# Optimization experiments

Measured on AMD Instinct MI355X. Metric: run time of the kernel, lower is better.

## Reference

```python
import jax, jax.numpy as jnp
import numpy as np

N_NODES = 50000
N_EDGES = 1600000
HIDDEN = 1024
NUM_CLASSES = 64


def setup_inputs() -> dict:
    key = jax.random.key(0)
    k1, k2, k3 = jax.random.split(key, 3)
    x = jax.random.normal(k1, (N_NODES, HIDDEN), dtype=jnp.float32)
    edge_index = jax.random.randint(k2, (2, N_EDGES), 0, N_NODES, dtype=jnp.int64)
    # Glorot-style init for the GCNConv linear weight, zero bias (PyG defaults)
    W = jax.random.normal(k3, (HIDDEN, NUM_CLASSES), dtype=jnp.float32) / np.sqrt(HIDDEN)
    b = jnp.zeros((NUM_CLASSES,), dtype=jnp.float32)
    return {"x": x, "edge_index": edge_index, "W": W, "b": b}


def reference(x, edge_index, W, b):
    # GCNConv: add self-loops, symmetric deg^{-1/2} normalization,
    # linear transform, gather-scale-scatter aggregation, bias, then softmax.
    n = x.shape[0]
    loops = jnp.arange(n, dtype=edge_index.dtype)
    src = jnp.concatenate([edge_index[0], loops])  # [E+N]
    dst = jnp.concatenate([edge_index[1], loops])  # [E+N]

    ones = jnp.ones(dst.shape[0], dtype=x.dtype)
    deg = jax.ops.segment_sum(ones, dst, num_segments=n)  # in-degree incl. self-loop
    deg_inv_sqrt = jnp.where(deg > 0, jax.lax.rsqrt(deg), 0.0)
    norm = deg_inv_sqrt[src] * deg_inv_sqrt[dst]  # [E+N]

    h = x @ W  # [N, C] dense GEMM (transform before propagate)
    msgs = h[src] * norm[:, None]  # gather + scale
    out = jax.ops.segment_sum(msgs, dst, num_segments=n) + b  # scatter-add
    return jax.nn.softmax(out, axis=1)
```

## Files before the change

kernel.cpp:

```cpp
#include <hip/hip_runtime.h>
#include <hip/hip_bf16.h>
#include <hip/hip_fp16.h>
#include <math.h>

#define HIDDEN 1024
#define NCLS 64
#define NB 196
#define BCAP 10240
#define CHUNK 4096
#define GCAP 4096
#define SMEM_BYTES 33280

typedef __attribute__((ext_vector_type(8))) short short8;
typedef __attribute__((ext_vector_type(4))) float f32x4;
typedef __attribute__((ext_vector_type(8))) _Float16 half8;

__device__ __forceinline__ short f2bf(float f) {
    __hip_bfloat16 b = __float2bfloat16(f);
    return __builtin_bit_cast(short, b);
}
__device__ __forceinline__ float bf2f(short s) {
    unsigned u = ((unsigned)(unsigned short)s) << 16;
    return __builtin_bit_cast(float, u);
}

__device__ __forceinline__ void async_copy16(void* lds, const void* g) {
    __builtin_amdgcn_global_load_lds(
        (const __attribute__((address_space(1))) unsigned int*)g,
        (__attribute__((address_space(3))) unsigned int*)lds, 16, 0, 0);
}

__global__ void wprep_kernel(const float* __restrict__ W,
                             short* __restrict__ wt_hi, short* __restrict__ wt_lo) {
    int idx = blockIdx.x * 256 + threadIdx.x;
    int c = idx >> 10;
    int k = idx & 1023;
    float f = W[(size_t)k * NCLS + c];
    short hb = f2bf(f);
    wt_hi[idx] = hb;
    wt_lo[idx] = f2bf(f - bf2f(hb));
}

__device__ void bucket_body(char* smem, const int* __restrict__ ei,
                            unsigned* __restrict__ pairs, int* __restrict__ bcnt,
                            int E, int bid) {
    int* hist = (int*)smem;
    int* offs = hist + 256;
    int* cur  = offs + 256;
    int* gbase = cur + 256;
    unsigned* stage = (unsigned*)(gbase + 256);
    int* nz = (int*)(stage + CHUNK);
    int* wsum = nz + 1;

    const int tid = threadIdx.x;
    const int base = bid * CHUNK;
    const int cnt_c = min(CHUNK, E - base);

    if (tid == 0) *nz = 0;
    hist[tid] = 0;
    cur[tid] = 0;
    __syncthreads();

    int found = 0;
    for (int j = tid; j < 1024; j += 256) {
        int e = base + j;
        if (e < E) found |= (ei[2 * e + 1] != 0);
    }
    if (found) atomicOr(nz, 1);
    __syncthreads();
    const int is64 = (*nz == 0);

    unsigned pr[16];
    #pragma unroll
    for (int j = 0; j < 16; ++j) {
        int e = base + j * 256 + tid;
        unsigned p = 0xFFFFFFFFu;
        if (e < E) {
            int s = is64 ? ei[2 * e] : ei[e];
            int d = is64 ? ei[2 * (E + e)] : ei[E + e];
            p = (unsigned)s | ((unsigned)d << 16);
            atomicAdd(&hist[d >> 8], 1);
        }
        pr[j] = p;
    }
    __syncthreads();

    int v = hist[tid];
    int incl = v;
    #pragma unroll
    for (int d = 1; d < 64; d <<= 1) {
        int t = __shfl_up(incl, d);
        if ((tid & 63) >= d) incl += t;
    }
    if ((tid & 63) == 63) wsum[tid >> 6] = incl;
    __syncthreads();
    int pre = 0;
    #pragma unroll
    for (int w = 0; w < 4; ++w)
        if (w < (tid >> 6)) pre += wsum[w];
    offs[tid] = pre + incl - v;
    if (tid < NB && v > 0) gbase[tid] = atomicAdd(&bcnt[tid], v);
    __syncthreads();

    #pragma unroll
    for (int j = 0; j < 16; ++j) {
        unsigned p = pr[j];
        if (p != 0xFFFFFFFFu) {
            int b = (int)(p >> 24);
            int pos = offs[b] + atomicAdd(&cur[b], 1);
            stage[pos] = p;
        }
    }
    __syncthreads();
    for (int i = tid; i < cnt_c; i += 256) {
        unsigned p = stage[i];
        int b = (int)(p >> 24);
        pairs[(size_t)b * BCAP + gbase[b] + (i - offs[b])] = p;
    }
}

__device__ void gemm_body(char* smem, const float* __restrict__ x,
                          const short* __restrict__ wt_hi, const short* __restrict__ wt_lo,
                          _Float16* __restrict__ h16, int M, int bid) {
    char* As = smem;
    char* Bh = smem + 16 * 1040;
    char* Bl = smem + 24 * 1040;

    const int tid = threadIdx.x;
    const int wave = tid >> 6;
    const int lane = tid & 63;
    const int l15 = lane & 15, l4 = lane >> 4;
    const int row0 = bid * 64;

    const float* agp[4];
    #pragma unroll
    for (int i = 0; i < 4; ++i) {
        int rg = row0 + (wave * 4 + i) * 4 + (lane >> 4);
        if (rg > M - 1) rg = M - 1;
        int g = (lane & 15) ^ (((lane >> 4) & 3) << 2);
        agp[i] = x + (size_t)rg * HIDDEN + g * 4;
    }
    const short* bhp[2];
    const short* blp[2];
    #pragma unroll
    for (int i = 0; i < 2; ++i) {
        int c = (wave * 2 + i) * 8 + (lane >> 3);
        int g = (lane & 7) ^ ((lane >> 3) & 7);
        bhp[i] = wt_hi + (size_t)c * HIDDEN + g * 8;
        blp[i] = wt_lo + (size_t)c * HIDDEN + g * 8;
    }

    f32x4 acc[4];
    #pragma unroll
    for (int nf = 0; nf < 4; ++nf) acc[nf] = (f32x4){0.f, 0.f, 0.f, 0.f};

    const int rt = wave * 16 + l15;
    const int r3 = rt & 3;
    char* arow = As + (rt >> 2) * 1040 + r3 * 256;

    for (int k0 = 0; k0 < HIDDEN; k0 += 64) {
        #pragma unroll
        for (int i = 0; i < 4; ++i)
            async_copy16(As + (wave * 4 + i) * 1040, agp[i] + k0);
        #pragma unroll
        for (int i = 0; i < 2; ++i) {
            async_copy16(Bh + (wave * 2 + i) * 1040, bhp[i] + k0);
            async_copy16(Bl + (wave * 2 + i) * 1040, blp[i] + k0);
        }
        __syncthreads();

        #pragma unroll
        for (int kk = 0; kk < 2; ++kk) {
            int js = (kk * 8 + l4 * 2) ^ (r3 << 2);
            f32x4 af0 = *reinterpret_cast<const f32x4*>(arow + js * 16);
            f32x4 af1 = *reinterpret_cast<const f32x4*>(arow + js * 16 + 16);
            short8 ah, al;
            #pragma unroll
            for (int j = 0; j < 4; ++j) {
                short hb = f2bf(af0[j]);
                ah[j] = hb;
                al[j] = f2bf(af0[j] - bf2f(hb));
                short hb2 = f2bf(af1[j]);
                ah[j + 4] = hb2;
                al[j + 4] = f2bf(af1[j] - bf2f(hb2));
            }
            #pragma unroll
            for (int nf = 0; nf < 4; ++nf) {
                int c = l15 + 16 * nf;
                int jb = (kk * 4 + l4) ^ (c & 7);
                size_t boff = (size_t)(c >> 3) * 1040 + (c & 7) * 128 + jb * 16;
                short8 bh = *reinterpret_cast<const short8*>(Bh + boff);
                short8 bl = *reinterpret_cast<const short8*>(Bl + boff);
                acc[nf] = __builtin_amdgcn_mfma_f32_16x16x32_bf16(ah, bh, acc[nf], 0, 0, 0);
                acc[nf] = __builtin_amdgcn_mfma_f32_16x16x32_bf16(al, bh, acc[nf], 0, 0, 0);
                acc[nf] = __builtin_amdgcn_mfma_f32_16x16x32_bf16(ah, bl, acc[nf], 0, 0, 0);
            }
        }
        __syncthreads();
    }

    #pragma unroll
    for (int j = 0; j < 4; ++j) {
        int r = row0 + wave * 16 + l4 * 4 + j;
        if (r < M) {
            #pragma unroll
            for (int nf = 0; nf < 4; ++nf) {
                h16[(size_t)r * NCLS + l15 + 16 * nf] = (_Float16)acc[nf][j];
            }
        }
    }
}

__global__ __launch_bounds__(256) void fat_kernel(const float* __restrict__ x,
                                                  const short* __restrict__ wt_hi,
                                                  const short* __restrict__ wt_lo,
                                                  _Float16* __restrict__ h16, int M,
                                                  const int* __restrict__ ei,
                                                  unsigned* __restrict__ pairs,
                                                  int* __restrict__ bcnt, int E,
                                                  int nGemmBlocks) {
    __shared__ __align__(16) char smem[SMEM_BYTES];
    if ((int)blockIdx.x < nGemmBlocks)
        gemm_body(smem, x, wt_hi, wt_lo, h16, M, blockIdx.x);
    else
        bucket_body(smem, ei, pairs, bcnt, E, blockIdx.x - nGemmBlocks);
}

__global__ __launch_bounds__(256) void degree_kernel(const unsigned* __restrict__ pairs,
                                                     const int* __restrict__ bcnt,
                                                     float* __restrict__ dis, int n) {
    __shared__ int hist[256];
    const int tid = threadIdx.x;
    const int bucket = blockIdx.x;
    hist[tid] = 0;
    __syncthreads();
    const int cb = bcnt[bucket];
    const unsigned* bp = pairs + (size_t)bucket * BCAP;
    for (int i = tid; i < cb; i += 256) {
        unsigned p = bp[i];
        atomicAdd(&hist[(p >> 16) & 255], 1);
    }
    __syncthreads();
    int node = bucket * 256 + tid;
    if (node < n) dis[node] = rsqrtf((float)hist[tid] + 1.0f);
}

__global__ __launch_bounds__(256) void agg_kernel(const unsigned* __restrict__ pairs,
                                                  const int* __restrict__ bcnt,
                                                  const _Float16* __restrict__ h16,
                                                  const float* __restrict__ dis,
                                                  const float* __restrict__ bias,
                                                  float* __restrict__ out, int n) {
    __shared__ int hist[64];
    __shared__ int offs[64];
    __shared__ int cur[64];
    __shared__ unsigned short ssrc[GCAP];
    __shared__ float swt[GCAP];
    const int tid = threadIdx.x;
    const int bucket = blockIdx.x >> 2;
    const int split = blockIdx.x & 3;
    const int base_node = bucket * 256 + split * 64;
    if (base_node >= n) return;
    if (tid < 64) { hist[tid] = 0; cur[tid] = 0; }
    __syncthreads();
    const int cb = bcnt[bucket];
    const unsigned* bp = pairs + (size_t)bucket * BCAP;
    for (int i = tid; i < cb; i += 256) {
        unsigned p = bp[i];
        int loc = (int)((p >> 16) & 255u);
        if ((loc >> 6) == split) atomicAdd(&hist[loc & 63], 1);
    }
    __syncthreads();
    if (tid == 0) {
        int r = 0;
        #pragma unroll
        for (int k = 0; k < 64; ++k) { offs[k] = r; r += hist[k]; }
    }
    __syncthreads();
    for (int i = tid; i < cb; i += 256) {
        unsigned p = bp[i];
        int loc = (int)((p >> 16) & 255u);
        if ((loc >> 6) == split) {
            int ln = loc & 63;
            int pos = offs[ln] + atomicAdd(&cur[ln], 1);
            if (pos < GCAP) {
                int s = (int)(p & 0xFFFFu);
                ssrc[pos] = (unsigned short)s;
                swt[pos] = dis[s];
            }
        }
    }
    __syncthreads();

    const int wave = tid >> 6;
    const int lane = tid & 63;
    const int q = lane & 7;
    const int g = lane >> 3;
    float bv[8];
    #pragma unroll
    for (int c = 0; c < 8; ++c) bv[c] = bias[q * 8 + c];

    for (int t = 0; t < 16; ++t) {
        int ln = wave * 16 + t;
        int node = base_node + ln;
        if (node >= n) continue;
        int len = hist[ln];
        int e0 = offs[ln];
        float di = rsqrtf((float)len + 1.0f);

        half8 hs = *reinterpret_cast<const half8*>(h16 + (size_t)node * NCLS + q * 8);
        float selfw = (g == 0) ? di : 0.f;
        float a[8], a2[8];
        #pragma unroll
        for (int c = 0; c < 8; ++c) { a[c] = (float)hs[c] * selfw; a2[c] = 0.f; }

        for (int i = 0; i < len; i += 16) {
            int i1 = i + g;
            bool v1 = i1 < len;
            int s1 = v1 ? (int)ssrc[e0 + i1] : 0;
            float w1 = v1 ? swt[e0 + i1] : 0.f;
            half8 r1 = *reinterpret_cast<const half8*>(h16 + (size_t)s1 * NCLS + q * 8);
            if (i + 8 < len) {
                int i2 = i + 8 + g;
                bool v2 = i2 < len;
                int s2 = v2 ? (int)ssrc[e0 + i2] : 0;
                float w2 = v2 ? swt[e0 + i2] : 0.f;
                half8 r2 = *reinterpret_cast<const half8*>(h16 + (size_t)s2 * NCLS + q * 8);
                #pragma unroll
                for (int c = 0; c < 8; ++c) a2[c] += w2 * (float)r2[c];
            }
            #pragma unroll
            for (int c = 0; c < 8; ++c) a[c] += w1 * (float)r1[c];
        }
        #pragma unroll
        for (int c = 0; c < 8; ++c) {
            float s = a[c] + a2[c];
            s += __shfl_xor(s, 8);
            s += __shfl_xor(s, 16);
            s += __shfl_xor(s, 32);
            a[c] = s * di + bv[c];
        }
        float m = a[0];
        #pragma unroll
        for (int c = 1; c < 8; ++c) m = fmaxf(m, a[c]);
        #pragma unroll
        for (int d = 1; d < 8; d <<= 1) m = fmaxf(m, __shfl_xor(m, d));
        float ex[8], sum = 0.f;
        #pragma unroll
        for (int c = 0; c < 8; ++c) { ex[c] = __expf(a[c] - m); sum += ex[c]; }
        #pragma unroll
        for (int d = 1; d < 8; d <<= 1) sum += __shfl_xor(sum, d);
        float inv = 1.f / sum;
        if (g == 0) {
            f32x4 o0 = {ex[0] * inv, ex[1] * inv, ex[2] * inv, ex[3] * inv};
            f32x4 o1 = {ex[4] * inv, ex[5] * inv, ex[6] * inv, ex[7] * inv};
            *reinterpret_cast<f32x4*>(out + (size_t)node * NCLS + q * 8) = o0;
            *reinterpret_cast<f32x4*>(out + (size_t)node * NCLS + q * 8 + 4) = o1;
        }
    }
}

extern "C" void kernel_launch(void* const* d_in, const int* in_sizes, int n_in,
                              void* d_out, int out_size, void* d_ws, size_t ws_size,
                              hipStream_t stream) {
    const float* x    = (const float*)d_in[0];
    const int*   ei   = (const int*)d_in[1];
    const float* W    = (const float*)d_in[2];
    const float* bias = (const float*)d_in[3];
    float* out = (float*)d_out;

    const int n = in_sizes[0] / HIDDEN;
    const int E = in_sizes[1] / 2;

    char* ws = (char*)d_ws;
    size_t off = 0;
    auto alloc = [&](size_t bytes) -> void* {
        void* p = (void*)(ws + off);
        off = (off + bytes + 255) & ~((size_t)255);
        return p;
    };
    int*      bcnt  = (int*)alloc((size_t)NB * 4);
    unsigned* pairs = (unsigned*)alloc((size_t)NB * BCAP * 4);
    float*    dis   = (float*)alloc((size_t)n * 4);
    _Float16* h16   = (_Float16*)alloc((size_t)n * NCLS * 2);
    short*    wt_hi = (short*)alloc((size_t)NCLS * HIDDEN * 2);
    short*    wt_lo = (short*)alloc((size_t)NCLS * HIDDEN * 2);
    (void)ws_size;

    hipMemsetAsync(bcnt, 0, (size_t)NB * 4, stream);

    wprep_kernel<<<(NCLS * HIDDEN) / 256, 256, 0, stream>>>(W, wt_hi, wt_lo);

    const int nGemmBlocks = (n + 63) / 64;
    const int nBucketBlocks = (E + CHUNK - 1) / CHUNK;
    fat_kernel<<<nGemmBlocks + nBucketBlocks, 256, 0, stream>>>(
        x, wt_hi, wt_lo, h16, n, ei, pairs, bcnt, E, nGemmBlocks);

    degree_kernel<<<NB, 256, 0, stream>>>(pairs, bcnt, dis, n);
    agg_kernel<<<NB * 4, 256, 0, stream>>>(pairs, bcnt, h16, dis, bias, out, n);
}
```

Before: 135.3 us.

## Bucket edges into 64-node groups so aggregation scans only its own pairs

The edge bucketing now sorts by destination into 784 buckets of 64 nodes instead of 196 buckets of 256 nodes. Each aggregation block reads only its own bucket rather than scanning a 256-node bucket four times and filtering, which cuts redundant pair reads and removes the shared-memory overflow guard. The GEMM part of the fused kernel also becomes a half-size grid where each block loops over two tiles. The trade-off is more global atomics and larger shared-memory histograms during bucketing, plus a tighter per-bucket capacity (2560) that could overflow on skewed degree distributions.

```diff
diff --git a/kernel.cpp b/kernel.cpp
--- a/kernel.cpp
+++ b/kernel.cpp
@@ -5,10 +5,9 @@
 
 #define HIDDEN 1024
 #define NCLS 64
-#define NB 196
-#define BCAP 10240
+#define NB2 784
+#define BCAP2 2560
 #define CHUNK 4096
-#define GCAP 4096
 #define SMEM_BYTES 33280
 
 typedef __attribute__((ext_vector_type(8))) short short8;
@@ -42,13 +41,13 @@
 }
 
 __device__ void bucket_body(char* smem, const int* __restrict__ ei,
-                            unsigned* __restrict__ pairs, int* __restrict__ bcnt,
+                            unsigned* __restrict__ pairs2, int* __restrict__ bcnt2,
                             int E, int bid) {
-    int* hist = (int*)smem;
-    int* offs = hist + 256;
-    int* cur  = offs + 256;
-    int* gbase = cur + 256;
-    unsigned* stage = (unsigned*)(gbase + 256);
+    int* hist  = (int*)smem;
+    int* offs  = hist + 1024;
+    int* cur   = offs + 1024;
+    int* gbase = cur + 1024;
+    unsigned* stage = (unsigned*)(gbase + 1024);
     int* nz = (int*)(stage + CHUNK);
     int* wsum = nz + 1;
 
@@ -57,8 +56,8 @@
     const int cnt_c = min(CHUNK, E - base);
 
     if (tid == 0) *nz = 0;
-    hist[tid] = 0;
-    cur[tid] = 0;
+    #pragma unroll
+    for (int j = 0; j < 4; ++j) { hist[tid + 256 * j] = 0; cur[tid + 256 * j] = 0; }
     __syncthreads();
 
     int found = 0;
@@ -79,18 +78,20 @@
             int s = is64 ? ei[2 * e] : ei[e];
             int d = is64 ? ei[2 * (E + e)] : ei[E + e];
             p = (unsigned)s | ((unsigned)d << 16);
-            atomicAdd(&hist[d >> 8], 1);
+            atomicAdd(&hist[d >> 6], 1);
         }
         pr[j] = p;
     }
     __syncthreads();
 
-    int v = hist[tid];
-    int incl = v;
+    const int b0 = 4 * tid;
+    int h0 = hist[b0], h1 = hist[b0 + 1], h2 = hist[b0 + 2], h3 = hist[b0 + 3];
+    int S = h0 + h1 + h2 + h3;
+    int incl = S;
     #pragma unroll
     for (int d = 1; d < 64; d <<= 1) {
-        int t = __shfl_up(incl, d);
-        if ((tid & 63) >= d) incl += t;
+        int t2 = __shfl_up(incl, d);
+        if ((tid & 63) >= d) incl += t2;
     }
     if ((tid & 63) == 63) wsum[tid >> 6] = incl;
     __syncthreads();
@@ -98,15 +99,22 @@
     #pragma unroll
     for (int w = 0; w < 4; ++w)
         if (w < (tid >> 6)) pre += wsum[w];
-    offs[tid] = pre + incl - v;
-    if (tid < NB && v > 0) gbase[tid] = atomicAdd(&bcnt[tid], v);
+    int ex = pre + incl - S;
+    offs[b0] = ex;
+    offs[b0 + 1] = ex + h0;
+    offs[b0 + 2] = ex + h0 + h1;
+    offs[b0 + 3] = ex + h0 + h1 + h2;
+    if (h0 > 0) gbase[b0] = atomicAdd(&bcnt2[b0], h0);
+    if (h1 > 0) gbase[b0 + 1] = atomicAdd(&bcnt2[b0 + 1], h1);
+    if (h2 > 0) gbase[b0 + 2] = atomicAdd(&bcnt2[b0 + 2], h2);
+    if (h3 > 0) gbase[b0 + 3] = atomicAdd(&bcnt2[b0 + 3], h3);
     __syncthreads();
 
     #pragma unroll
     for (int j = 0; j < 16; ++j) {
         unsigned p = pr[j];
         if (p != 0xFFFFFFFFu) {
-            int b = (int)(p >> 24);
+            int b = (int)(p >> 22);
             int pos = offs[b] + atomicAdd(&cur[b], 1);
             stage[pos] = p;
         }
@@ -114,8 +122,8 @@
     __syncthreads();
     for (int i = tid; i < cnt_c; i += 256) {
         unsigned p = stage[i];
-        int b = (int)(p >> 24);
-        pairs[(size_t)b * BCAP + gbase[b] + (i - offs[b])] = p;
+        int b = (int)(p >> 22);
+        pairs2[(size_t)b * BCAP2 + gbase[b] + (i - offs[b])] = p;
     }
 }
 
@@ -216,37 +224,41 @@
                                                   const short* __restrict__ wt_lo,
                                                   _Float16* __restrict__ h16, int M,
                                                   const int* __restrict__ ei,
-                                                  unsigned* __restrict__ pairs,
-                                                  int* __restrict__ bcnt, int E,
-                                                  int nGemmBlocks) {
+                                                  unsigned* __restrict__ pairs2,
+                                                  int* __restrict__ bcnt2, int E,
+                                                  int nGemmGrid, int nTiles) {
     __shared__ __align__(16) char smem[SMEM_BYTES];
-    if ((int)blockIdx.x < nGemmBlocks)
-        gemm_body(smem, x, wt_hi, wt_lo, h16, M, blockIdx.x);
-    else
-        bucket_body(smem, ei, pairs, bcnt, E, blockIdx.x - nGemmBlocks);
-}
-
-__global__ __launch_bounds__(256) void degree_kernel(const unsigned* __restrict__ pairs,
-                                                     const int* __restrict__ bcnt,
+    const int bid = blockIdx.x;
+    if (bid < nGemmGrid) {
+        for (int t = bid; t < nTiles; t += nGemmGrid)
+            gemm_body(smem, x, wt_hi, wt_lo, h16, M, t);
+    } else {
+        bucket_body(smem, ei, pairs2, bcnt2, E, bid - nGemmGrid);
+    }
+}
+
+__global__ __launch_bounds__(256) void degree_kernel(const unsigned* __restrict__ pairs2,
+                                                     const int* __restrict__ bcnt2,
                                                      float* __restrict__ dis, int n) {
     __shared__ int hist[256];
     const int tid = threadIdx.x;
-    const int bucket = blockIdx.x;
     hist[tid] = 0;
     __syncthreads();
-    const int cb = bcnt[bucket];
-    const unsigned* bp = pairs + (size_t)bucket * BCAP;
-    for (int i = tid; i < cb; i += 256) {
-        unsigned p = bp[i];
-        atomicAdd(&hist[(p >> 16) & 255], 1);
-    }
-    __syncthreads();
-    int node = bucket * 256 + tid;
+    #pragma unroll
+    for (int gg = 0; gg < 4; ++gg) {
+        int g = blockIdx.x * 4 + gg;
+        const int cb = bcnt2[g];
+        const unsigned* bp = pairs2 + (size_t)g * BCAP2;
+        for (int i = tid; i < cb; i += 256)
+            atomicAdd(&hist[gg * 64 + ((bp[i] >> 16) & 63)], 1);
+    }
+    __syncthreads();
+    int node = blockIdx.x * 256 + tid;
     if (node < n) dis[node] = rsqrtf((float)hist[tid] + 1.0f);
 }
 
-__global__ __launch_bounds__(256) void agg_kernel(const unsigned* __restrict__ pairs,
-                                                  const int* __restrict__ bcnt,
+__global__ __launch_bounds__(256) void agg_kernel(const unsigned* __restrict__ pairs2,
+                                                  const int* __restrict__ bcnt2,
                                                   const _Float16* __restrict__ h16,
                                                   const float* __restrict__ dis,
                                                   const float* __restrict__ bias,
@@ -254,41 +266,32 @@
     __shared__ int hist[64];
     __shared__ int offs[64];
     __shared__ int cur[64];
-    __shared__ unsigned short ssrc[GCAP];
-    __shared__ float swt[GCAP];
+    __shared__ unsigned short ssrc[BCAP2];
+    __shared__ float swt[BCAP2];
     const int tid = threadIdx.x;
-    const int bucket = blockIdx.x >> 2;
-    const int split = blockIdx.x & 3;
-    const int base_node = bucket * 256 + split * 64;
+    const int grp = blockIdx.x;
+    const int base_node = grp * 64;
     if (base_node >= n) return;
     if (tid < 64) { hist[tid] = 0; cur[tid] = 0; }
     __syncthreads();
-    const int cb = bcnt[bucket];
-    const unsigned* bp = pairs + (size_t)bucket * BCAP;
+    const int cb = bcnt2[grp];
+    const unsigned* bp = pairs2 + (size_t)grp * BCAP2;
+    for (int i = tid; i < cb; i += 256)
+        atomicAdd(&hist[(bp[i] >> 16) & 63], 1);
+    __syncthreads();
+    if (tid == 0) {
+        int r = 0;
+        #pragma unroll
+        for (int k = 0; k < 64; ++k) { offs[k] = r; r += hist[k]; }
+    }
+    __syncthreads();
     for (int i = tid; i < cb; i += 256) {
         unsigned p = bp[i];
-        int loc = (int)((p >> 16) & 255u);
-        if ((loc >> 6) == split) atomicAdd(&hist[loc & 63], 1);
-    }
-    __syncthreads();
-    if (tid == 0) {
-        int r = 0;
-        #pragma unroll
-        for (int k = 0; k < 64; ++k) { offs[k] = r; r += hist[k]; }
-    }
-    __syncthreads();
-    for (int i = tid; i < cb; i += 256) {
-        unsigned p = bp[i];
-        int loc = (int)((p >> 16) & 255u);
-        if ((loc >> 6) == split) {
-            int ln = loc & 63;
-            int pos = offs[ln] + atomicAdd(&cur[ln], 1);
-            if (pos < GCAP) {
-                int s = (int)(p & 0xFFFFu);
-                ssrc[pos] = (unsigned short)s;
-                swt[pos] = dis[s];
-            }
-        }
+        int ln = (p >> 16) & 63;
+        int pos = offs[ln] + atomicAdd(&cur[ln], 1);
+        int s = (int)(p & 0xFFFFu);
+        ssrc[pos] = (unsigned short)s;
+        swt[pos] = dis[s];
     }
     __syncthreads();
 
@@ -379,23 +382,25 @@
         off = (off + bytes + 255) & ~((size_t)255);
         return p;
     };
-    int*      bcnt  = (int*)alloc((size_t)NB * 4);
-    unsigned* pairs = (unsigned*)alloc((size_t)NB * BCAP * 4);
-    float*    dis   = (float*)alloc((size_t)n * 4);
-    _Float16* h16   = (_Float16*)alloc((size_t)n * NCLS * 2);
-    short*    wt_hi = (short*)alloc((size_t)NCLS * HIDDEN * 2);
-    short*    wt_lo = (short*)alloc((size_t)NCLS * HIDDEN * 2);
+    int*      bcnt2  = (int*)alloc((size_t)NB2 * 4);
+    unsigned* pairs2 = (unsigned*)alloc((size_t)NB2 * BCAP2 * 4);
+    float*    dis    = (float*)alloc((size_t)n * 4);
+    _Float16* h16    = (_Float16*)alloc((size_t)n * NCLS * 2);
+    short*    wt_hi  = (short*)alloc((size_t)NCLS * HIDDEN * 2);
+    short*    wt_lo  = (short*)alloc((size_t)NCLS * HIDDEN * 2);
     (void)ws_size;
 
-    hipMemsetAsync(bcnt, 0, (size_t)NB * 4, stream);
+    hipMemsetAsync(bcnt2, 0, (size_t)NB2 * 4, stream);
 
     wprep_kernel<<<(NCLS * HIDDEN) / 256, 256, 0, stream>>>(W, wt_hi, wt_lo);
 
-    const int nGemmBlocks = (n + 63) / 64;
+    const int nTiles = (n + 63) / 64;
+    const int nGemmGrid = (nTiles + 1) / 2;
     const int nBucketBlocks = (E + CHUNK - 1) / CHUNK;
-    fat_kernel<<<nGemmBlocks + nBucketBlocks, 256, 0, stream>>>(
-        x, wt_hi, wt_lo, h16, n, ei, pairs, bcnt, E, nGemmBlocks);
-
-    degree_kernel<<<NB, 256, 0, stream>>>(pairs, bcnt, dis, n);
-    agg_kernel<<<NB * 4, 256, 0, stream>>>(pairs, bcnt, h16, dis, bias, out, n);
-}
+    fat_kernel<<<nGemmGrid + nBucketBlocks, 256, 0, stream>>>(
+        x, wt_hi, wt_lo, h16, n, ei, pairs2, bcnt2, E, nGemmGrid, nTiles);
+
+    const int nGroups = (n + 63) / 64;
+    degree_kernel<<<(nGroups + 3) / 4, 256, 0, stream>>>(pairs2, bcnt2, dis, n);
+    agg_kernel<<<nGroups, 256, 0, stream>>>(pairs2, bcnt2, h16, dis, bias, out, n);
+}
```

Measured after the change: 146.0 us. 7.9% more time.
